# Kernel tuning notes

Measured on AMD Instinct MI355X. Metric: run time of the kernel, lower is better.

The kernel has to match this reference:

```python
import jax, jax.numpy as jnp
import numpy as np

EPS = 1e-5

def layer_norm(x, w, b):
    mu = jnp.mean(x, axis=-1, keepdims=True)
    var = jnp.mean(jnp.square(x - mu), axis=-1, keepdims=True)
    return (x - mu) * jax.lax.rsqrt(var + EPS) * w + b

def setup_inputs() -> dict:
    key = jax.random.key(0)
    k1, k2, k3, k4, k5, k6 = jax.random.split(key, 6)
    d = 768
    q_x = jax.random.normal(k1, (1, 8, d), dtype=jnp.float32)
    kv_x = jax.random.normal(k2, (32, 196, d), dtype=jnp.float32)
    ln_q_w = 1.0 + 0.1 * jax.random.normal(k3, (d,), dtype=jnp.float32)
    ln_q_b = 0.1 * jax.random.normal(k4, (d,), dtype=jnp.float32)
    ln_kv_w = 1.0 + 0.1 * jax.random.normal(k5, (d,), dtype=jnp.float32)
    ln_kv_b = 0.1 * jax.random.normal(k6, (d,), dtype=jnp.float32)
    return {"q_x": q_x, "kv_x": kv_x, "ln_q_w": ln_q_w, "ln_q_b": ln_q_b,
            "ln_kv_w": ln_kv_w, "ln_kv_b": ln_kv_b}

def reference(q_x, kv_x, ln_q_w, ln_q_b, ln_kv_w, ln_kv_b):
    b, n_patch, d = kv_x.shape
    n_q = q_x.shape[1]
    # expanded q is identical across b^2 rows -> normalize the single copy
    qn = layer_norm(q_x, ln_q_w, ln_q_b)[0]          # (n_q, d)
    kvn = layer_norm(kv_x, ln_kv_w, ln_kv_b)         # (b, n_patch, d)
    # pairwise batch differences: (b, b, n_patch, d) -> (b^2, n_patch, d)
    kv_pair = (kvn[:, None] - kvn[None, :]).reshape(b * b, n_patch, d)
    scores = jnp.einsum('qd,pnd->pqn', qn, kv_pair) / jnp.sqrt(jnp.asarray(d, qn.dtype))
    attn = jax.nn.softmax(scores, axis=-1)           # (b^2, n_q, n_patch)
    values = jnp.einsum('pqn,pnd->pqd', attn, kv_pair)
    return values
```

## Files before the change

### kernel.cpp

```cpp
#include <hip/hip_runtime.h>
#include <math.h>

constexpr int D  = 768;
constexpr int NQ = 8;
constexpr int B  = 32;
constexpr int NP = 196;
constexpr int KT = 7;
constexpr int KP = KT * 32;
constexpr int TPAD = 776;
constexpr int NTOFF = 28;
constexpr int NTILES = 32;
constexpr float EPS = 1e-5f;
constexpr float INV_SQRT_D = 0.036084391824351615f;

typedef __attribute__((ext_vector_type(8))) short short8;
typedef __attribute__((ext_vector_type(4))) float f32x4;

__device__ __forceinline__ float wave_reduce_sum(float v) {
#pragma unroll
    for (int off = 32; off > 0; off >>= 1) v += __shfl_xor(v, off, 64);
    return v;
}
__device__ __forceinline__ float wave_reduce_max(float v) {
#pragma unroll
    for (int off = 32; off > 0; off >>= 1) v = fmaxf(v, __shfl_xor(v, off, 64));
    return v;
}

__device__ __forceinline__ unsigned short f2bf(float x) {
    union { float f; unsigned u; } c; c.f = x;
    unsigned r = c.u + 0x7fffu + ((c.u >> 16) & 1u);
    return (unsigned short)(r >> 16);
}

__global__ __launch_bounds__(256) void kv_fused(const float* __restrict__ q_x,
                                                const float* __restrict__ qw,
                                                const float* __restrict__ qb,
                                                const float* __restrict__ kv_x,
                                                const float* __restrict__ kw,
                                                const float* __restrict__ kb,
                                                float* __restrict__ S,
                                                unsigned short* __restrict__ kvTf) {
    const int b = blockIdx.x / 14;
    const int h = blockIdx.x % 14;
    const int kt = h >> 1;
    const int kgbase = (h & 1) * 2;
    const int tid = threadIdx.x, wave = tid >> 6, lane = tid & 63;
    __shared__ unsigned short tile[16][TPAD];
    __shared__ unsigned short qbf[16][TPAD];

    const bool live = (h * 16) < NP;

    float wv[12], bv[12];
#pragma unroll
    for (int c = 0; c < 12; ++c) { wv[c] = kw[lane + 64 * c]; bv[c] = kb[lane + 64 * c]; }

    if (live && wave < 4) {
        float wq[12], bq[12];
#pragma unroll
        for (int c = 0; c < 12; ++c) { wq[c] = qw[lane + 64 * c]; bq[c] = qb[lane + 64 * c]; }
        for (int rr = 0; rr < 2; ++rr) {
            const int q = wave * 2 + rr;
            float v[12];
            float s = 0.f;
#pragma unroll
            for (int c = 0; c < 12; ++c) { v[c] = q_x[q * D + lane + 64 * c]; s += v[c]; }
            s = wave_reduce_sum(s);
            const float mean = s * (1.0f / D);
            float ss = 0.f;
#pragma unroll
            for (int c = 0; c < 12; ++c) { v[c] -= mean; ss += v[c] * v[c]; }
            ss = wave_reduce_sum(ss);
            const float rs = rsqrtf(ss * (1.0f / D) + EPS);
#pragma unroll
            for (int c = 0; c < 12; ++c)
                qbf[q][lane + 64 * c] = f2bf(v[c] * rs * wq[c] + bq[c]);
        }
    }

    for (int r = 0; r < 4; ++r) {
        const int nl = wave * 4 + r;
        const int n  = h * 16 + nl;
        if (n < NP) {
            const float* xr = kv_x + ((size_t)b * NP + n) * D;
            float v[12];
            float s = 0.f;
#pragma unroll
            for (int c = 0; c < 12; ++c) { v[c] = xr[lane + 64 * c]; s += v[c]; }
            s = wave_reduce_sum(s);
            const float mean = s * (1.0f / D);
            float ss = 0.f;
#pragma unroll
            for (int c = 0; c < 12; ++c) { v[c] -= mean; ss += v[c] * v[c]; }
            ss = wave_reduce_sum(ss);
            const float rs = rsqrtf(ss * (1.0f / D) + EPS);
#pragma unroll
            for (int c = 0; c < 12; ++c)
                tile[nl][lane + 64 * c] = f2bf(v[c] * rs * wv[c] + bv[c]);
        } else {
#pragma unroll
            for (int c = 0; c < 12; ++c) tile[nl][lane + 64 * c] = 0;
        }
    }
    __syncthreads();

#pragma unroll
    for (int rep = 0; rep < 6; ++rep) {
        const int chunk = rep * 256 + tid;
        const int dt = chunk >> 5, ls = chunk & 31;
        const int hi = ls >> 4, dl = ls & 15;
        const int kg = kgbase + hi;
        short8 vals;
#pragma unroll
        for (int e = 0; e < 8; ++e)
            vals[e] = (short)tile[hi * 8 + e][dt * 16 + dl];
        *(short8*)(kvTf + ((((size_t)b * 48 + dt) * KT + kt) * 64 + kg * 16 + dl) * 8) = vals;
    }

    if (live && wave == 0) {
        f32x4 s0 = {0.f, 0.f, 0.f, 0.f}, s1 = {0.f, 0.f, 0.f, 0.f};
        const int ar = lane & 15, akg = lane >> 4;
#pragma unroll
        for (int k2 = 0; k2 < 24; k2 += 2) {
            s0 = __builtin_amdgcn_mfma_f32_16x16x32_bf16(
                *(const short8*)&tile[ar][k2 * 32 + akg * 8],
                *(const short8*)&qbf[ar][k2 * 32 + akg * 8], s0, 0, 0, 0);
            s1 = __builtin_amdgcn_mfma_f32_16x16x32_bf16(
                *(const short8*)&tile[ar][(k2 + 1) * 32 + akg * 8],
                *(const short8*)&qbf[ar][(k2 + 1) * 32 + akg * 8], s1, 0, 0, 0);
        }
        s0 = s0 + s1;
        const int q = lane & 15;
        if (q < NQ) {
#pragma unroll
            for (int reg = 0; reg < 4; ++reg) {
                const int n = h * 16 + akg * 4 + reg;
                if (n < NP) S[((size_t)b * NQ + q) * NP + n] = s0[reg] * INV_SQRT_D;
            }
        }
    }
}

__global__ __launch_bounds__(512) void aprep(const float* __restrict__ S,
                                             unsigned short* __restrict__ Abf) {
    const int u = blockIdx.x;
    int uu = u, i = 0;
    while (uu >= 31 - i) { uu -= 31 - i; ++i; }
    const int j = i + 1 + uu;

    const int tid = threadIdx.x, wave = tid >> 6, lane = tid & 63;
    __shared__ unsigned short lrow[16][KP];

    for (int jj = 0; jj < 2; ++jj) {
        const int r = wave * 2 + jj;
        const int dir = r >> 3, q = r & 7;
        const float* Sa = S + ((size_t)(dir ? j : i) * NQ + q) * NP;
        const float* Sb = S + ((size_t)(dir ? i : j) * NQ + q) * NP;
        float v[4];
        float m = -1e30f;
#pragma unroll
        for (int c = 0; c < 4; ++c) {
            const int n = lane + 64 * c;
            v[c] = (n < NP) ? (Sa[n] - Sb[n]) : -1e30f;
            m = fmaxf(m, v[c]);
        }
        m = wave_reduce_max(m);
        float e[4];
        float sum = 0.f;
#pragma unroll
        for (int c = 0; c < 4; ++c) {
            const int n = lane + 64 * c;
            e[c] = (n < NP) ? __expf(v[c] - m) : 0.f;
            sum += e[c];
        }
        sum = wave_reduce_sum(sum);
        const float rinv = 1.0f / sum;
#pragma unroll
        for (int c = 0; c < 4; ++c) {
            const int n = lane + 64 * c;
            if (n < KP) lrow[r][n] = (n < NP) ? f2bf(e[c] * rinv) : (unsigned short)0;
        }
    }
    __syncthreads();

    if (tid < 448) {
        const int kt = tid >> 6, slot = tid & 63;
        const int kg = slot >> 4, lr = slot & 15;
        const short8 vals = *(const short8*)(&lrow[lr][kt * 32 + kg * 8]);
        *(short8*)(Abf + (((size_t)u * KT + kt) * 64 + slot) * 8) = vals;
    }
}

__global__ __launch_bounds__(1024) void dgemm(const unsigned short* __restrict__ Abf,
                                              const unsigned short* __restrict__ kvTf,
                                              float* __restrict__ out) {
    const int bid = blockIdx.x;
    const int t = bid >> 3, cs = bid & 7;
    const int tid = threadIdx.x, wave = tid >> 6, lane = tid & 63;

    __shared__ unsigned short stg[2][8][6][64][8];

    const bool offd = (t < NTOFF);
    int gi = 0, gj = 0;
    if (offd) {
        int tt = t, a = 0;
        while (tt >= 7 - a) { tt -= 7 - a; ++a; }
        gi = a; gj = a + 1 + tt;
    }
    const int dbase = 8 * (t - NTOFF);

    int i0 = 0, j0 = 0, i1 = 0, j1 = 0;
    int p0i = 0, p0j = 0, p1i = 0, p1j = 0, dth = 0;
    bool compute = true;
    if (offd) {
        const int pi = wave >> 2, bh = (wave >> 1) & 1;
        dth = wave & 1;
        i0 = 4 * gi + pi; j0 = 4 * gj + 2 * bh;
        i1 = i0;          j1 = j0 + 1;
        p0i = pi; p0j = 4 + 2 * bh; p1i = pi; p1j = p0j + 1;
    } else if (wave < 12) {
        const int ps = wave >> 1;
        dth = wave & 1;
        const int g = ps / 3, k3 = ps - 3 * g;
        const int ea[6] = {0, 0, 0, 1, 1, 2}, eb[6] = {1, 2, 3, 2, 3, 3};
        const int e0 = 2 * k3, e1 = e0 + 1;
        p0i = 4 * g + ea[e0]; p0j = 4 * g + eb[e0];
        p1i = 4 * g + ea[e1]; p1j = 4 * g + eb[e1];
        i0 = dbase + p0i; j0 = dbase + p0j;
        i1 = dbase + p1i; j1 = dbase + p1j;
    } else {
        compute = false;
        const int zw = wave - 12;
#pragma unroll
        for (int t2 = 0; t2 < 2; ++t2) {
            const int ii = dbase + zw * 2 + t2;
            float* base = out + (size_t)(ii * B + ii) * NQ * D + cs * 96;
            for (int e = lane; e < NQ * 96; e += 64) {
                const int q = e / 96, c = e - q * 96;
                base[q * D + c] = 0.f;
            }
        }
    }

    short8 areg0[KT], areg1[KT];
    if (compute) {
        const int u0 = (i0 * (63 - i0)) / 2 + (j0 - i0 - 1);
        const int u1 = (i1 * (63 - i1)) / 2 + (j1 - i1 - 1);
        const unsigned short* Au0 = Abf + (size_t)u0 * KT * 512 + (size_t)lane * 8;
        const unsigned short* Au1 = Abf + (size_t)u1 * KT * 512 + (size_t)lane * 8;
#pragma unroll
        for (int kt = 0; kt < KT; ++kt) {
            areg0[kt] = *(const short8*)(Au0 + (size_t)kt * 512);
            areg1[kt] = *(const short8*)(Au1 + (size_t)kt * 512);
        }
    }

    const int sp = wave >> 1;
    const int sd0 = (wave & 1) * 3;
    const int sb = offd ? ((sp < 4) ? (4 * gi + sp) : (4 * gj + sp - 4)) : (dbase + sp);
    const unsigned short* gbase =
        kvTf + (((size_t)sb * 48 + cs * 6 + sd0) * KT) * 512 + (size_t)lane * 8;

    f32x4 acc0[3], acc1[3];
#pragma unroll
    for (int nf = 0; nf < 3; ++nf) {
        f32x4 z = {0.f, 0.f, 0.f, 0.f};
        acc0[nf] = z; acc1[nf] = z;
    }

#pragma unroll
    for (int r = 0; r < 3; ++r)
        __builtin_amdgcn_global_load_lds(
            (const __attribute__((address_space(1))) void*)(gbase + ((size_t)r * KT) * 512),
            (__attribute__((address_space(3))) void*)(&stg[0][sp][sd0 + r][0][0]), 16, 0, 0);
    __syncthreads();

    int buf = 0;
    for (int kt = 0; kt < KT; ++kt) {
        if (kt + 1 < KT) {
#pragma unroll
            for (int r = 0; r < 3; ++r)
                __builtin_amdgcn_global_load_lds(
                    (const __attribute__((address_space(1))) void*)(gbase + ((size_t)r * KT + kt + 1) * 512),
                    (__attribute__((address_space(3))) void*)(&stg[buf ^ 1][sp][sd0 + r][0][0]), 16, 0, 0);
        }
        if (compute) {
            const short8 a0 = areg0[kt], a1 = areg1[kt];
            short8 na0, na1;
#pragma unroll
            for (int e = 0; e < 8; ++e) {
                na0[e] = (short)(a0[e] ^ (short)0x8000);
                na1[e] = (short)(a1[e] ^ (short)0x8000);
            }
            if (offd) {
#pragma unroll
                for (int nf = 0; nf < 3; ++nf) {
                    const short8 ki  = *(const short8*)(&stg[buf][p0i][dth * 3 + nf][lane][0]);
                    const short8 kj0 = *(const short8*)(&stg[buf][p0j][dth * 3 + nf][lane][0]);
                    const short8 kj1 = *(const short8*)(&stg[buf][p1j][dth * 3 + nf][lane][0]);
                    acc0[nf] = __builtin_amdgcn_mfma_f32_16x16x32_bf16(a0,  ki,  acc0[nf], 0, 0, 0);
                    acc0[nf] = __builtin_amdgcn_mfma_f32_16x16x32_bf16(na0, kj0, acc0[nf], 0, 0, 0);
                    acc1[nf] = __builtin_amdgcn_mfma_f32_16x16x32_bf16(a1,  ki,  acc1[nf], 0, 0, 0);
                    acc1[nf] = __builtin_amdgcn_mfma_f32_16x16x32_bf16(na1, kj1, acc1[nf], 0, 0, 0);
                }
            } else {
#pragma unroll
                for (int nf = 0; nf < 3; ++nf) {
                    const short8 k0i = *(const short8*)(&stg[buf][p0i][dth * 3 + nf][lane][0]);
                    const short8 k0j = *(const short8*)(&stg[buf][p0j][dth * 3 + nf][lane][0]);
                    const short8 k1i = *(const short8*)(&stg[buf][p1i][dth * 3 + nf][lane][0]);
                    const short8 k1j = *(const short8*)(&stg[buf][p1j][dth * 3 + nf][lane][0]);
                    acc0[nf] = __builtin_amdgcn_mfma_f32_16x16x32_bf16(a0,  k0i, acc0[nf], 0, 0, 0);
                    acc0[nf] = __builtin_amdgcn_mfma_f32_16x16x32_bf16(na0, k0j, acc0[nf], 0, 0, 0);
                    acc1[nf] = __builtin_amdgcn_mfma_f32_16x16x32_bf16(a1,  k1i, acc1[nf], 0, 0, 0);
                    acc1[nf] = __builtin_amdgcn_mfma_f32_16x16x32_bf16(na1, k1j, acc1[nf], 0, 0, 0);
                }
            }
        }
        __syncthreads();
        buf ^= 1;
    }

    if (compute) {
        const int kgrp = lane >> 4, dl = lane & 15;
        const int colb = cs * 96 + dth * 48 + dl;
#pragma unroll
        for (int pr = 0; pr < 2; ++pr) {
            const int i = pr ? i1 : i0, j = pr ? j1 : j0;
            const f32x4* acc = pr ? acc1 : acc0;
            const int pij = i * B + j, pji = j * B + i;
#pragma unroll
            for (int reg = 0; reg < 4; ++reg) {
                const int r = kgrp * 4 + reg;
                const int dirr = r >> 3, qq = r & 7;
                const int p = dirr ? pji : pij;
                const float sgn = dirr ? -1.f : 1.f;
                float* op = out + ((size_t)p * NQ + qq) * D + colb;
#pragma unroll
                for (int nf = 0; nf < 3; ++nf) op[nf * 16] = sgn * acc[nf][reg];
            }
        }
    }
}

extern "C" void kernel_launch(void* const* d_in, const int* in_sizes, int n_in,
                              void* d_out, int out_size, void* d_ws, size_t ws_size,
                              hipStream_t stream) {
    const float* q_x     = (const float*)d_in[0];
    const float* kv_x    = (const float*)d_in[1];
    const float* ln_q_w  = (const float*)d_in[2];
    const float* ln_q_b  = (const float*)d_in[3];
    const float* ln_kv_w = (const float*)d_in[4];
    const float* ln_kv_b = (const float*)d_in[5];
    float* out = (float*)d_out;

    float* ws = (float*)d_ws;
    float* S  = ws;
    unsigned short* kvTf = (unsigned short*)(ws + B * NQ * NP);
    unsigned short* Abf  = kvTf + (size_t)B * 48 * KT * 512;

    kv_fused<<<B * 14, 256, 0, stream>>>(q_x, ln_q_w, ln_q_b, kv_x, ln_kv_w, ln_kv_b, S, kvTf);
    aprep<<<(B * (B - 1)) / 2, 512, 0, stream>>>(S, Abf);
    dgemm<<<NTILES * 8, 1024, 0, stream>>>(Abf, kvTf, out);
}
```

Baseline: 38.77 us.

## Retile pairwise-difference GEMM into 8x4 batch-pair blocks with streamed A operands

```diff
diff --git a/kernel.cpp b/kernel.cpp
--- a/kernel.cpp
+++ b/kernel.cpp
@@ -8,8 +8,7 @@
 constexpr int KT = 7;
 constexpr int KP = KT * 32;
 constexpr int TPAD = 776;
-constexpr int NTOFF = 28;
-constexpr int NTILES = 32;
+constexpr int CS = 24;
 constexpr float EPS = 1e-5f;
 constexpr float INV_SQRT_D = 0.036084391824351615f;
 
@@ -33,21 +32,21 @@
     return (unsigned short)(r >> 16);
 }
 
-__global__ __launch_bounds__(256) void kv_fused(const float* __restrict__ q_x,
-                                                const float* __restrict__ qw,
-                                                const float* __restrict__ qb,
-                                                const float* __restrict__ kv_x,
-                                                const float* __restrict__ kw,
-                                                const float* __restrict__ kb,
-                                                float* __restrict__ S,
-                                                unsigned short* __restrict__ kvTf) {
+__global__ __launch_bounds__(256, 4) void kv_fused(const float* __restrict__ q_x,
+                                                   const float* __restrict__ qw,
+                                                   const float* __restrict__ qb,
+                                                   const float* __restrict__ kv_x,
+                                                   const float* __restrict__ kw,
+                                                   const float* __restrict__ kb,
+                                                   float* __restrict__ S,
+                                                   unsigned short* __restrict__ kvTf) {
     const int b = blockIdx.x / 14;
     const int h = blockIdx.x % 14;
     const int kt = h >> 1;
     const int kgbase = (h & 1) * 2;
     const int tid = threadIdx.x, wave = tid >> 6, lane = tid & 63;
     __shared__ unsigned short tile[16][TPAD];
-    __shared__ unsigned short qbf[16][TPAD];
+    __shared__ unsigned short qbf[8][TPAD];
 
     const bool live = (h * 16) < NP;
 
@@ -120,14 +119,15 @@
     if (live && wave == 0) {
         f32x4 s0 = {0.f, 0.f, 0.f, 0.f}, s1 = {0.f, 0.f, 0.f, 0.f};
         const int ar = lane & 15, akg = lane >> 4;
+        const int qr = ar & 7;
 #pragma unroll
         for (int k2 = 0; k2 < 24; k2 += 2) {
             s0 = __builtin_amdgcn_mfma_f32_16x16x32_bf16(
                 *(const short8*)&tile[ar][k2 * 32 + akg * 8],
-                *(const short8*)&qbf[ar][k2 * 32 + akg * 8], s0, 0, 0, 0);
+                *(const short8*)&qbf[qr][k2 * 32 + akg * 8], s0, 0, 0, 0);
             s1 = __builtin_amdgcn_mfma_f32_16x16x32_bf16(
                 *(const short8*)&tile[ar][(k2 + 1) * 32 + akg * 8],
-                *(const short8*)&qbf[ar][(k2 + 1) * 32 + akg * 8], s1, 0, 0, 0);
+                *(const short8*)&qbf[qr][(k2 + 1) * 32 + akg * 8], s1, 0, 0, 0);
         }
         s0 = s0 + s1;
         const int q = lane & 15;
@@ -191,153 +191,156 @@
     }
 }
 
-__global__ __launch_bounds__(1024) void dgemm(const unsigned short* __restrict__ Abf,
-                                              const unsigned short* __restrict__ kvTf,
-                                              float* __restrict__ out) {
+__global__ __launch_bounds__(256) void dgemm(const unsigned short* __restrict__ Abf,
+                                             const unsigned short* __restrict__ kvTf,
+                                             float* __restrict__ out) {
     const int bid = blockIdx.x;
-    const int t = bid >> 3, cs = bid & 7;
+    const int cs = bid % CS, bt = bid / CS;
     const int tid = threadIdx.x, wave = tid >> 6, lane = tid & 63;
 
-    __shared__ unsigned short stg[2][8][6][64][8];
-
-    const bool offd = (t < NTOFF);
-    int gi = 0, gj = 0;
-    if (offd) {
-        int tt = t, a = 0;
-        while (tt >= 7 - a) { tt -= 7 - a; ++a; }
-        gi = a; gj = a + 1 + tt;
-    }
-    const int dbase = 8 * (t - NTOFF);
-
-    int i0 = 0, j0 = 0, i1 = 0, j1 = 0;
-    int p0i = 0, p0j = 0, p1i = 0, p1j = 0, dth = 0;
-    bool compute = true;
-    if (offd) {
-        const int pi = wave >> 2, bh = (wave >> 1) & 1;
-        dth = wave & 1;
-        i0 = 4 * gi + pi; j0 = 4 * gj + 2 * bh;
-        i1 = i0;          j1 = j0 + 1;
-        p0i = pi; p0j = 4 + 2 * bh; p1i = pi; p1j = p0j + 1;
-    } else if (wave < 12) {
-        const int ps = wave >> 1;
-        dth = wave & 1;
-        const int g = ps / 3, k3 = ps - 3 * g;
-        const int ea[6] = {0, 0, 0, 1, 1, 2}, eb[6] = {1, 2, 3, 2, 3, 3};
-        const int e0 = 2 * k3, e1 = e0 + 1;
-        p0i = 4 * g + ea[e0]; p0j = 4 * g + eb[e0];
-        p1i = 4 * g + ea[e1]; p1j = 4 * g + eb[e1];
-        i0 = dbase + p0i; j0 = dbase + p0j;
-        i1 = dbase + p1i; j1 = dbase + p1j;
+    __shared__ unsigned short stg[2][12][2][64][8];
+
+    const bool rect = bt < 12;
+    int ib0, jb0, jpanb, g8 = 0, jh = 0;
+    if (rect) {
+        const int ft = bt >> 1;
+        jh = bt & 1;
+        const int gA = (ft < 3) ? 0 : ((ft < 5) ? 1 : 2);
+        const int gB = (ft < 3) ? (ft + 1) : ((ft < 5) ? (ft - 1) : 3);
+        ib0 = 8 * gA; jb0 = 8 * gB + 4 * jh; jpanb = 8;
     } else {
-        compute = false;
-        const int zw = wave - 12;
-#pragma unroll
-        for (int t2 = 0; t2 < 2; ++t2) {
-            const int ii = dbase + zw * 2 + t2;
-            float* base = out + (size_t)(ii * B + ii) * NQ * D + cs * 96;
-            for (int e = lane; e < NQ * 96; e += 64) {
-                const int q = e / 96, c = e - q * 96;
-                base[q * D + c] = 0.f;
-            }
-        }
-    }
-
-    short8 areg0[KT], areg1[KT];
+        g8 = (bt - 12) >> 1; jh = (bt - 12) & 1;
+        ib0 = 8 * g8; jb0 = 8 * g8 + 4 * jh; jpanb = 4 * jh;
+    }
+
+    int ig[2], jg[4];
+    ig[0] = ib0 + 2 * wave; ig[1] = ig[0] + 1;
+#pragma unroll
+    for (int jj = 0; jj < 4; ++jj) jg[jj] = jb0 + jj;
+    bool valid[8];
+    bool any = false;
+#pragma unroll
+    for (int p = 0; p < 8; ++p) {
+        valid[p] = ig[p >> 2] < jg[p & 3];
+        any = any || valid[p];
+    }
+    const bool compute = any;
+
+    if (!rect && jh == 0 && wave >= 2) {
+#pragma unroll
+        for (int t2 = 0; t2 < 4; ++t2) {
+            const int ii = ib0 + (wave - 2) * 4 + t2;
+            float* base = out + (size_t)(ii * B + ii) * NQ * D + cs * 32;
+            const int col = lane & 31, qh = lane >> 5;
+#pragma unroll
+            for (int rr = 0; rr < 4; ++rr)
+                base[(qh * 4 + rr) * D + col] = 0.f;
+        }
+    }
+
+    const unsigned short* Ap[8];
+#pragma unroll
+    for (int p = 0; p < 8; ++p) {
+        const int i = ig[p >> 2], j = jg[p & 3];
+        const int u = valid[p] ? (i * (63 - i)) / 2 + (j - i - 1) : 0;
+        Ap[p] = Abf + (size_t)u * KT * 512 + (size_t)lane * 8;
+    }
+
+    short8 acur[8], anxt[8];
     if (compute) {
-        const int u0 = (i0 * (63 - i0)) / 2 + (j0 - i0 - 1);
-        const int u1 = (i1 * (63 - i1)) / 2 + (j1 - i1 - 1);
-        const unsigned short* Au0 = Abf + (size_t)u0 * KT * 512 + (size_t)lane * 8;
-        const unsigned short* Au1 = Abf + (size_t)u1 * KT * 512 + (size_t)lane * 8;
-#pragma unroll
-        for (int kt = 0; kt < KT; ++kt) {
-            areg0[kt] = *(const short8*)(Au0 + (size_t)kt * 512);
-            areg1[kt] = *(const short8*)(Au1 + (size_t)kt * 512);
-        }
-    }
-
-    const int sp = wave >> 1;
-    const int sd0 = (wave & 1) * 3;
-    const int sb = offd ? ((sp < 4) ? (4 * gi + sp) : (4 * gj + sp - 4)) : (dbase + sp);
-    const unsigned short* gbase =
-        kvTf + (((size_t)sb * 48 + cs * 6 + sd0) * KT) * 512 + (size_t)lane * 8;
-
-    f32x4 acc0[3], acc1[3];
-#pragma unroll
-    for (int nf = 0; nf < 3; ++nf) {
-        f32x4 z = {0.f, 0.f, 0.f, 0.f};
-        acc0[nf] = z; acc1[nf] = z;
-    }
-
-#pragma unroll
-    for (int r = 0; r < 3; ++r)
+#pragma unroll
+        for (int p = 0; p < 8; ++p) acur[p] = *(const short8*)(Ap[p]);
+    }
+
+    const int nst = rect ? 6 : 4;
+    int sb[6], sdt[6], spn[6];
+#pragma unroll
+    for (int s = 0; s < 6; ++s) {
+        const int unit = wave * nst + s;
+        const int p = unit >> 1, dt = unit & 1;
+        spn[s] = p; sdt[s] = dt;
+        sb[s] = rect ? ((p < 8) ? (ib0 + p) : (jb0 + (p - 8))) : (ib0 + p);
+    }
+
+    f32x4 acc[8][2];
+#pragma unroll
+    for (int p = 0; p < 8; ++p)
+#pragma unroll
+        for (int dt = 0; dt < 2; ++dt) {
+            f32x4 z = {0.f, 0.f, 0.f, 0.f};
+            acc[p][dt] = z;
+        }
+
+    for (int s = 0; s < nst; ++s)
         __builtin_amdgcn_global_load_lds(
-            (const __attribute__((address_space(1))) void*)(gbase + ((size_t)r * KT) * 512),
-            (__attribute__((address_space(3))) void*)(&stg[0][sp][sd0 + r][0][0]), 16, 0, 0);
+            (const __attribute__((address_space(1))) void*)(
+                kvTf + (((size_t)sb[s] * 48 + cs * 2 + sdt[s]) * KT) * 512 + (size_t)lane * 8),
+            (__attribute__((address_space(3))) void*)(&stg[0][spn[s]][sdt[s]][0][0]), 16, 0, 0);
     __syncthreads();
 
     int buf = 0;
     for (int kt = 0; kt < KT; ++kt) {
         if (kt + 1 < KT) {
-#pragma unroll
-            for (int r = 0; r < 3; ++r)
+            for (int s = 0; s < nst; ++s)
                 __builtin_amdgcn_global_load_lds(
-                    (const __attribute__((address_space(1))) void*)(gbase + ((size_t)r * KT + kt + 1) * 512),
-                    (__attribute__((address_space(3))) void*)(&stg[buf ^ 1][sp][sd0 + r][0][0]), 16, 0, 0);
+                    (const __attribute__((address_space(1))) void*)(
+                        kvTf + (((size_t)sb[s] * 48 + cs * 2 + sdt[s]) * KT + kt + 1) * 512 + (size_t)lane * 8),
+                    (__attribute__((address_space(3))) void*)(&stg[buf ^ 1][spn[s]][sdt[s]][0][0]), 16, 0, 0);
+            if (compute) {
+#pragma unroll
+                for (int p = 0; p < 8; ++p) anxt[p] = *(const short8*)(Ap[p] + (size_t)(kt + 1) * 512);
+            }
         }
         if (compute) {
-            const short8 a0 = areg0[kt], a1 = areg1[kt];
-            short8 na0, na1;
-#pragma unroll
-            for (int e = 0; e < 8; ++e) {
-                na0[e] = (short)(a0[e] ^ (short)0x8000);
-                na1[e] = (short)(a1[e] ^ (short)0x8000);
+            const int il0 = 2 * wave;
+#pragma unroll
+            for (int dt = 0; dt < 2; ++dt) {
+                const short8 ki0 = *(const short8*)(&stg[buf][il0][dt][lane][0]);
+                const short8 ki1 = *(const short8*)(&stg[buf][il0 + 1][dt][lane][0]);
+                short8 nkj[4];
+#pragma unroll
+                for (int jj = 0; jj < 4; ++jj) {
+                    const short8 kj = *(const short8*)(&stg[buf][jpanb + jj][dt][lane][0]);
+#pragma unroll
+                    for (int e = 0; e < 8; ++e) nkj[jj][e] = (short)(kj[e] ^ (short)0x8000);
+                }
+#pragma unroll
+                for (int ii2 = 0; ii2 < 2; ++ii2)
+#pragma unroll
+                    for (int jj = 0; jj < 4; ++jj) {
+                        const int p = ii2 * 4 + jj;
+                        acc[p][dt] = __builtin_amdgcn_mfma_f32_16x16x32_bf16(
+                            acur[p], ii2 ? ki1 : ki0, acc[p][dt], 0, 0, 0);
+                        acc[p][dt] = __builtin_amdgcn_mfma_f32_16x16x32_bf16(
+                            acur[p], nkj[jj], acc[p][dt], 0, 0, 0);
+                    }
             }
-            if (offd) {
-#pragma unroll
-                for (int nf = 0; nf < 3; ++nf) {
-                    const short8 ki  = *(const short8*)(&stg[buf][p0i][dth * 3 + nf][lane][0]);
-                    const short8 kj0 = *(const short8*)(&stg[buf][p0j][dth * 3 + nf][lane][0]);
-                    const short8 kj1 = *(const short8*)(&stg[buf][p1j][dth * 3 + nf][lane][0]);
-                    acc0[nf] = __builtin_amdgcn_mfma_f32_16x16x32_bf16(a0,  ki,  acc0[nf], 0, 0, 0);
-                    acc0[nf] = __builtin_amdgcn_mfma_f32_16x16x32_bf16(na0, kj0, acc0[nf], 0, 0, 0);
-                    acc1[nf] = __builtin_amdgcn_mfma_f32_16x16x32_bf16(a1,  ki,  acc1[nf], 0, 0, 0);
-                    acc1[nf] = __builtin_amdgcn_mfma_f32_16x16x32_bf16(na1, kj1, acc1[nf], 0, 0, 0);
-                }
-            } else {
-#pragma unroll
-                for (int nf = 0; nf < 3; ++nf) {
-                    const short8 k0i = *(const short8*)(&stg[buf][p0i][dth * 3 + nf][lane][0]);
-                    const short8 k0j = *(const short8*)(&stg[buf][p0j][dth * 3 + nf][lane][0]);
-                    const short8 k1i = *(const short8*)(&stg[buf][p1i][dth * 3 + nf][lane][0]);
-                    const short8 k1j = *(const short8*)(&stg[buf][p1j][dth * 3 + nf][lane][0]);
-                    acc0[nf] = __builtin_amdgcn_mfma_f32_16x16x32_bf16(a0,  k0i, acc0[nf], 0, 0, 0);
-                    acc0[nf] = __builtin_amdgcn_mfma_f32_16x16x32_bf16(na0, k0j, acc0[nf], 0, 0, 0);
-                    acc1[nf] = __builtin_amdgcn_mfma_f32_16x16x32_bf16(a1,  k1i, acc1[nf], 0, 0, 0);
-                    acc1[nf] = __builtin_amdgcn_mfma_f32_16x16x32_bf16(na1, k1j, acc1[nf], 0, 0, 0);
-                }
-            }
         }
         __syncthreads();
+        if (compute && kt + 1 < KT) {
+#pragma unroll
+            for (int p = 0; p < 8; ++p) acur[p] = anxt[p];
+        }
         buf ^= 1;
     }
 
     if (compute) {
         const int kgrp = lane >> 4, dl = lane & 15;
-        const int colb = cs * 96 + dth * 48 + dl;
-#pragma unroll
-        for (int pr = 0; pr < 2; ++pr) {
-            const int i = pr ? i1 : i0, j = pr ? j1 : j0;
-            const f32x4* acc = pr ? acc1 : acc0;
-            const int pij = i * B + j, pji = j * B + i;
-#pragma unroll
-            for (int reg = 0; reg < 4; ++reg) {
-                const int r = kgrp * 4 + reg;
-                const int dirr = r >> 3, qq = r & 7;
-                const int p = dirr ? pji : pij;
-                const float sgn = dirr ? -1.f : 1.f;
-                float* op = out + ((size_t)p * NQ + qq) * D + colb;
-#pragma unroll
-                for (int nf = 0; nf < 3; ++nf) op[nf * 16] = sgn * acc[nf][reg];
+#pragma unroll
+        for (int p = 0; p < 8; ++p) {
+            if (valid[p]) {
+                const int i = ig[p >> 2], j = jg[p & 3];
+                const int pij = i * B + j, pji = j * B + i;
+#pragma unroll
+                for (int reg = 0; reg < 4; ++reg) {
+                    const int r = kgrp * 4 + reg;
+                    const int dirr = r >> 3, qq = r & 7;
+                    const int po = dirr ? pji : pij;
+                    const float sgn = dirr ? -1.f : 1.f;
+                    float* op = out + ((size_t)po * NQ + qq) * D + cs * 32 + dl;
+                    op[0]  = sgn * acc[p][0][reg];
+                    op[16] = sgn * acc[p][1][reg];
+                }
             }
         }
     }
@@ -361,5 +364,5 @@
 
     kv_fused<<<B * 14, 256, 0, stream>>>(q_x, ln_q_w, ln_q_b, kv_x, ln_kv_w, ln_kv_b, S, kvTf);
     aprep<<<(B * (B - 1)) / 2, 512, 0, stream>>>(S, Abf);
-    dgemm<<<NTILES * 8, 1024, 0, stream>>>(Abf, kvTf, out);
-}
+    dgemm<<<20 * CS, 256, 0, stream>>>(Abf, kvTf, out);
+}
```

New measurement: 44.63 us. +15.1%, slower.
